# Performance work log

Measured on AMD Instinct MI355X. Metric: run time of the kernel, lower is better.

## Reference

```python
import jax, jax.numpy as jnp
import numpy as np

NUM_HEADS = 12


def setup_inputs() -> dict:
    key = jax.random.key(0)
    k1, k2, k3 = jax.random.split(key, 3)
    B, T, N, D = 8, 8, 196, 768
    x = jax.random.normal(k1, (B, T * N, D), dtype=jnp.float32)
    w_qkv = jax.random.normal(k2, (D, 3 * D), dtype=jnp.float32) * 0.02
    w_proj = jax.random.normal(k3, (D, D), dtype=jnp.float32) * 0.02
    b_proj = jnp.zeros((D,), dtype=jnp.float32)
    return {"x": x, "T": T, "N": N, "w_qkv": w_qkv, "w_proj": w_proj, "b_proj": b_proj}


def reference(x, T, N, w_qkv, w_proj, b_proj):
    B, TN, D = x.shape
    H = NUM_HEADS
    hd = D // H
    scale = hd ** -0.5
    # qkv projection: (B, TN, 3, H, hd)
    qkv = (x @ w_qkv).reshape(B, TN, 3, H, hd)
    # -> (3, B, H, T, N, hd)
    qkv = jnp.transpose(qkv, (2, 0, 3, 1, 4)).reshape(3, B, H, T, N, hd)
    q, k, v = qkv[0], qkv[1], qkv[2]

    # Temporal branch: mean-pool over spatial axis N (keepdim -> length-1 attn axis)
    q_t = q.mean(axis=3, keepdims=True)            # (B,H,T,1,hd)
    k_t = k.mean(axis=3, keepdims=True)            # (B,H,T,1,hd)
    v_t = v.mean(axis=3, keepdims=True)            # (B,H,T,1,hd)
    attn_t = jnp.einsum('bhtqd,bhtkd->bhtqk', q_t, k_t) * scale  # (B,H,T,1,1)
    attn_t = jax.nn.softmax(attn_t, axis=-1)
    x_t = jnp.einsum('bhtqk,bhtkd->bhtqd', attn_t, v_t)[:, :, :, 0]  # (B,H,T,hd)

    # Spatial branch: full attention within each frame
    attn_s = jnp.einsum('bhtnd,bhtmd->bhtnm', q, k) * scale  # (B,H,T,N,N)
    attn_s = jax.nn.softmax(attn_s, axis=-1)
    x_s = jnp.einsum('bhtnm,bhtmd->bhtnd', attn_s, v)        # (B,H,T,N,hd)

    # Combine: broadcast temporal result over spatial positions, add
    out = x_s + x_t[:, :, :, None, :]                        # (B,H,T,N,hd)
    out = out.reshape(B, H, T * N, hd)
    out = jnp.transpose(out, (0, 2, 1, 3)).reshape(B * T * N, D)
    return out @ w_proj + b_proj
```

## Files before the change

kernel.cpp:

```cpp
#include <hip/hip_runtime.h>
#include <math.h>

#define BB 8
#define TT 8
#define NN 196
#define DD 768
#define HH 12
#define HD 64
#define TN (TT * NN)
#define MM (BB * TN)
#define D3 (3 * DD)

typedef _Float16 f16;
typedef _Float16 f16x8 __attribute__((ext_vector_type(8)));
typedef _Float16 f16x4 __attribute__((ext_vector_type(4)));
typedef float f32x4 __attribute__((ext_vector_type(4)));
typedef unsigned int u32;

#define GLDS16(gp, lp)                                                        \
  __builtin_amdgcn_global_load_lds(                                           \
      (const __attribute__((address_space(1))) u32*)(gp),                     \
      (__attribute__((address_space(3))) u32*)(lp), 16, 0, 0)

#define MFMA16(a, b, c) __builtin_amdgcn_mfma_f32_16x16x32_f16(a, b, c, 0, 0, 0)
#define SBAR() __builtin_amdgcn_s_barrier()
#define SCHED() __builtin_amdgcn_sched_barrier(0)
#define PBAR()  do { SCHED(); SBAR(); SCHED(); } while (0)

#define GK DD
#define GNT 12

template <int MI0, int NJ0>
__device__ __forceinline__ void quad(f32x4 (&acc)[8][4],
                                     const f16x8 (&af)[4][2],
                                     const f16x8 (&bf)[2][2]) {
  __builtin_amdgcn_s_setprio(1);
#pragma unroll
  for (int i = 0; i < 4; i++)
#pragma unroll
    for (int j = 0; j < 2; j++) {
      acc[MI0 + i][NJ0 + j] = MFMA16(af[i][0], bf[j][0], acc[MI0 + i][NJ0 + j]);
      acc[MI0 + i][NJ0 + j] = MFMA16(af[i][1], bf[j][1], acc[MI0 + i][NJ0 + j]);
    }
  __builtin_amdgcn_s_setprio(0);
}

__global__ __launch_bounds__(512, 2) void gemm256_qkv(
    const f16* __restrict__ A, const f16* __restrict__ Bt,
    f16* __restrict__ C16) {
  __shared__ f16 As[2 * 256 * 64];
  __shared__ f16 Bs[2 * 256 * 64];

  const int nwg = 49 * 9;
  const int orig = blockIdx.x;
  const int xcd = orig & 7;
  const int inner = orig >> 3;
  const int qq = nwg >> 3;
  const int rr = nwg & 7;
  const int swzid =
      ((xcd < rr) ? xcd * (qq + 1) : rr * (qq + 1) + (xcd - rr) * qq) + inner;
  const int bm = (swzid / 9) * 256;
  const int bn = (swzid % 9) * 256;

  const int tid = threadIdx.x;
  const int lane = tid & 63;
  const int wave = tid >> 6;
  const int wy = wave >> 2;
  const int wx = wave & 3;
  const int m = lane & 15;
  const int q = lane >> 4;

  const int sr = tid >> 3;
  const int sc = (tid & 7) ^ (sr & 7);
  const f16* gA = A + (size_t)(bm + sr) * GK + sc * 8;
  const f16* gB = Bt + (size_t)(bn + sr) * GK + sc * 8;
  f16* lA = &As[tid * 8];
  f16* lB = &Bs[tid * 8];

#define STAGE_A(db, h, tile)                                   \
  do {                                                         \
    const f16* _s = gA + (size_t)(h) * 128 * GK + (tile) * 64; \
    f16* _d = lA + (db) * 16384 + (h) * 8192;                  \
    GLDS16(_s, _d);                                            \
    GLDS16(_s + 64 * GK, _d + 4096);                           \
  } while (0)
#define STAGE_B(db, h, tile)                                   \
  do {                                                         \
    const f16* _s = gB + (size_t)(h) * 128 * GK + (tile) * 64; \
    f16* _d = lB + (db) * 16384 + (h) * 8192;                  \
    GLDS16(_s, _d);                                            \
    GLDS16(_s + 64 * GK, _d + 4096);                           \
  } while (0)

  const int sw = m & 7;
  const int c0 = (q ^ sw) * 8;
  const int c1 = ((q + 4) ^ sw) * 8;
  const f16* rA = &As[(wy * 128 + m) * 64];
  const f16* rB = &Bs[(wx * 64 + m) * 64];

  STAGE_A(0, 0, 0);
  STAGE_A(0, 1, 0);
  STAGE_B(0, 0, 0);
  STAGE_B(0, 1, 0);
  STAGE_B(1, 0, 1);
  STAGE_B(1, 1, 1);

  f32x4 acc[8][4];
#pragma unroll
  for (int i = 0; i < 8; i++)
#pragma unroll
    for (int j = 0; j < 4; j++) acc[i][j] = (f32x4)0.0f;

  SCHED();
  asm volatile("s_waitcnt vmcnt(4)" ::: "memory");
  SCHED();
  SBAR();
  SCHED();

#pragma unroll 2
  for (int t = 0; t < GNT; ++t) {
    const int db = t & 1;
    const f16* pA = rA + db * 16384;
    const f16* pB = rB + db * 16384;
    const int tA = (t + 1 < GNT) ? t + 1 : GNT - 1;
    const int tB = (t + 2 < GNT) ? t + 2 : GNT - 1;

    f16x8 af[4][2], bf0[2][2], bf1[2][2];

#pragma unroll
    for (int i = 0; i < 4; i++) {
      af[i][0] = *(const f16x8*)(pA + i * 1024 + c0);
      af[i][1] = *(const f16x8*)(pA + i * 1024 + c1);
    }
#pragma unroll
    for (int j = 0; j < 2; j++) {
      bf0[j][0] = *(const f16x8*)(pB + j * 1024 + c0);
      bf0[j][1] = *(const f16x8*)(pB + j * 1024 + c1);
    }
    STAGE_A(db ^ 1, 0, tA);
    PBAR();
    quad<0, 0>(acc, af, bf0);
    PBAR();

#pragma unroll
    for (int j = 0; j < 2; j++) {
      bf1[j][0] = *(const f16x8*)(pB + (2 + j) * 1024 + c0);
      bf1[j][1] = *(const f16x8*)(pB + (2 + j) * 1024 + c1);
    }
    STAGE_A(db ^ 1, 1, tA);
    PBAR();
    quad<0, 2>(acc, af, bf1);
    PBAR();

#pragma unroll
    for (int i = 0; i < 4; i++) {
      af[i][0] = *(const f16x8*)(pA + (4 + i) * 1024 + c0);
      af[i][1] = *(const f16x8*)(pA + (4 + i) * 1024 + c1);
    }
    STAGE_B(db, 0, tB);
    PBAR();
    quad<4, 2>(acc, af, bf1);
    PBAR();

    STAGE_B(db, 1, tB);
    SCHED();
    asm volatile("s_waitcnt vmcnt(4)" ::: "memory");
    PBAR();
    quad<4, 0>(acc, af, bf0);
    PBAR();
  }

  const int col0 = bn + wx * 64;
#pragma unroll
  for (int mi = 0; mi < 8; mi++) {
    const int row0 = bm + wy * 128 + mi * 16 + q * 4;
#pragma unroll
    for (int r = 0; r < 4; r++) {
      const int token = row0 + r;
      const int f = token / NN;
      const int n = token - f * NN;
      f16* fb = C16 + ((size_t)f * (HH * 3)) * (NN * 64) + n * 64;
#pragma unroll
      for (int ni = 0; ni < 4; ni++) {
        const int col = col0 + ni * 16 + m;
        const int qt = col / DD;
        const int rem = col - qt * DD;
        const int hh = rem >> 6;
        const int d = rem & 63;
        fb[(size_t)(hh * 3 + qt) * (NN * 64) + d] = (f16)acc[mi][ni][r];
      }
    }
  }
#undef STAGE_A
#undef STAGE_B
}

__global__ __launch_bounds__(256) void gemm_f16nt(
    const f16* __restrict__ A, const f16* __restrict__ Bt,
    float* __restrict__ C32, f16* __restrict__ C16, int K, int Ncol,
    const float* __restrict__ bias, int mode) {
  __shared__ f16 As[128 * 64];
  __shared__ f16 Bs[128 * 64];

  const int tid = threadIdx.x;
  const int lane = tid & 63;
  const int wave = tid >> 6;
  const int wy = wave >> 1, wx = wave & 1;
  const int bm = blockIdx.y * 128;
  const int bn = blockIdx.x * 128;

  const f16* aP[4];
  const f16* bP[4];
#pragma unroll
  for (int it = 0; it < 4; it++) {
    int ci = tid + it * 256;
    int r = ci >> 3;
    int c = (ci & 7) ^ (r & 7);
    aP[it] = A + (size_t)(bm + r) * K + c * 8;
    bP[it] = Bt + (size_t)(bn + r) * K + c * 8;
  }

  f32x4 acc[4][4];
#pragma unroll
  for (int i = 0; i < 4; i++)
#pragma unroll
    for (int j = 0; j < 4; j++) acc[i][j] = (f32x4)0.0f;

  const int fr = lane & 15;
  const int q = lane >> 4;
  const int sw = fr & 7;

  for (int kt = 0; kt < K; kt += 64) {
#pragma unroll
    for (int it = 0; it < 4; it++) {
      GLDS16(aP[it] + kt, &As[(tid + it * 256) * 8]);
      GLDS16(bP[it] + kt, &Bs[(tid + it * 256) * 8]);
    }
    __syncthreads();

#pragma unroll
    for (int kk = 0; kk < 2; kk++) {
      const int lc = ((kk * 4 + q) ^ sw) * 8;
      f16x8 af[4], bf[4];
#pragma unroll
      for (int mi = 0; mi < 4; mi++)
        af[mi] = *(const f16x8*)&As[(wy * 64 + mi * 16 + fr) * 64 + lc];
#pragma unroll
      for (int ni = 0; ni < 4; ni++)
        bf[ni] = *(const f16x8*)&Bs[(wx * 64 + ni * 16 + fr) * 64 + lc];

#pragma unroll
      for (int mi = 0; mi < 4; mi++)
#pragma unroll
        for (int ni = 0; ni < 4; ni++)
          acc[mi][ni] = MFMA16(af[mi], bf[ni], acc[mi][ni]);
    }
    __syncthreads();
  }

  if (mode == 0) {
#pragma unroll
    for (int mi = 0; mi < 4; mi++) {
      const int row0 = bm + wy * 64 + mi * 16 + (lane >> 4) * 4;
#pragma unroll
      for (int ni = 0; ni < 4; ni++) {
        const int col = bn + wx * 64 + ni * 16 + (lane & 15);
        float bv = (bias != nullptr) ? bias[col] : 0.0f;
#pragma unroll
        for (int r = 0; r < 4; r++)
          C32[(size_t)(row0 + r) * Ncol + col] = acc[mi][ni][r] + bv;
      }
    }
  } else {
#pragma unroll
    for (int mi = 0; mi < 4; mi++) {
      const int row0 = bm + wy * 64 + mi * 16 + (lane >> 4) * 4;
#pragma unroll
      for (int r = 0; r < 4; r++) {
        const int token = row0 + r;
        const int f = token / NN;
        const int n = token - f * NN;
        f16* fb = C16 + ((size_t)f * (HH * 3) * NN) * 64 + n * 64;
#pragma unroll
        for (int ni = 0; ni < 4; ni++) {
          const int col = bn + wx * 64 + ni * 16 + (lane & 15);
          const int qt = col / DD;
          const int rem = col - qt * DD;
          const int hh = rem >> 6;
          const int d = rem & 63;
          fb[(size_t)(hh * 3 + qt) * NN * 64 + d] = (f16)acc[mi][ni][r];
        }
      }
    }
  }
}

__global__ __launch_bounds__(256) void conv_f32_to_f16(
    const float* __restrict__ in, f16* __restrict__ out, int n4) {
  int i = blockIdx.x * blockDim.x + threadIdx.x;
  const int stride = gridDim.x * blockDim.x;
  for (; i < n4; i += stride) {
    float4 f = ((const float4*)in)[i];
    f16x4 h;
    h[0] = (f16)f.x;
    h[1] = (f16)f.y;
    h[2] = (f16)f.z;
    h[3] = (f16)f.w;
    ((f16x4*)out)[i] = h;
  }
}

__global__ __launch_bounds__(256) void transpose_f32_to_f16(
    const float* __restrict__ W, f16* __restrict__ Wt, int K, int Ncol) {
  __shared__ float tileS[32][33];
  const int k0 = blockIdx.y * 32, n0 = blockIdx.x * 32;
  const int tx = threadIdx.x & 31, ty = threadIdx.x >> 5;
#pragma unroll
  for (int i = 0; i < 4; i++)
    tileS[ty + i * 8][tx] = W[(size_t)(k0 + ty + i * 8) * Ncol + n0 + tx];
  __syncthreads();
#pragma unroll
  for (int i = 0; i < 4; i++)
    Wt[(size_t)(n0 + ty + i * 8) * K + k0 + tx] = (f16)tileS[tx][ty + i * 8];
}

#define VSTR 232

__global__ __launch_bounds__(512, 4) void attn_mfma(
    const f16* __restrict__ qkv, f16* __restrict__ out) {
  __shared__ f16 KS[196 * 64];
  __shared__ f16 VS[64 * VSTR];
  __shared__ __align__(16) f16 PS[8 * 16 * 40];
  __shared__ float vmean[64];
  float* red = (float*)PS;

  const int bi = blockIdx.x;
  const int t = bi % TT;
  const int h = (bi / TT) % HH;
  const int b = bi / (TT * HH);
  const int frame = b * TT + t;
  const int tok0 = frame * NN;

  const f16* Qb = qkv + (size_t)(frame * HH + h) * 3 * NN * 64;
  const f16* Kb = Qb + NN * 64;
  const f16* Vb = Qb + 2 * NN * 64;

  const int tid = threadIdx.x;
  const int lane = tid & 63;
  const int wave = tid >> 6;
  const int m = lane & 15;
  const int q = lane >> 4;

#pragma unroll
  for (int it = 0; it < 3; it++) {
    int chunk = tid + it * 512;
    int row = chunk >> 3, pc = chunk & 7;
    int c = pc ^ (row & 7);
    GLDS16(Kb + row * 64 + c * 8, &KS[chunk * 8]);
  }
  if (tid < 32) {
    int chunk = 1536 + tid;
    int row = chunk >> 3, pc = chunk & 7;
    int c = pc ^ (row & 7);
    *(f16x8*)&KS[chunk * 8] = *(const f16x8*)(Kb + row * 64 + c * 8);
  }

  for (int idx = tid; idx < 64 * 9; idx += 512) {
    int d = idx / 9, c = idx % 9;
    *(f16x4*)&VS[d * VSTR + 196 + c * 4] = (f16x4){0, 0, 0, 0};
  }

  const int vd = tid & 63;
  const int kb = tid >> 6;
  float vpart = 0.0f;
  if (kb < 7) {
#pragma unroll
    for (int it = 0; it < 7; it++) {
      int k0 = kb * 28 + it * 4;
      f16x4 pk;
#pragma unroll
      for (int j = 0; j < 4; j++) {
        f16 v = Vb[(k0 + j) * 64 + vd];
        pk[j] = v;
        vpart += (float)v;
      }
      *(f16x4*)&VS[vd * VSTR + k0] = pk;
    }
  }
  red[tid] = vpart;
  __syncthreads();
  if (tid < 64) {
    float s = 0.0f;
#pragma unroll
    for (int g = 0; g < 8; g++) s += red[tid + 64 * g];
    vmean[tid] = s * (1.0f / (float)NN);
  }
  __syncthreads();

  f16* PSw = &PS[wave * 640];

  for (int qt = wave; qt < 13; qt += 8) {
    const int q0 = qt * 16;
    int qrow = q0 + m;
    if (qrow > NN - 1) qrow = NN - 1;
    const f16* qbase = Qb + qrow * 64;
    f16x8 aq0 = *(const f16x8*)(qbase + q * 8);
    f16x8 aq1 = *(const f16x8*)(qbase + 32 + q * 8);

    f32x4 o0 = (f32x4)0.0f, o1 = (f32x4)0.0f, o2 = (f32x4)0.0f,
          o3 = (f32x4)0.0f;
    float l[4] = {0.0f, 0.0f, 0.0f, 0.0f};

    for (int ch = 0; ch < 7; ch++) {
      const int keyA = ch * 32 + m;
      const int keyB = keyA + 16;
      const int kA = keyA > 195 ? 195 : keyA;
      const int kB = keyB > 195 ? 195 : keyB;
      const int swA = kA & 7, swB = kB & 7;
      f16x8 b00 = *(const f16x8*)&KS[kA * 64 + ((q ^ swA) * 8)];
      f16x8 b01 = *(const f16x8*)&KS[kA * 64 + (((q + 4) ^ swA) * 8)];
      f16x8 b10 = *(const f16x8*)&KS[kB * 64 + ((q ^ swB) * 8)];
      f16x8 b11 = *(const f16x8*)&KS[kB * 64 + (((q + 4) ^ swB) * 8)];
      f32x4 z = (f32x4)0.0f;
      f32x4 s0 = MFMA16(aq0, b00, z);
      s0 = MFMA16(aq1, b01, s0);
      f32x4 s1 = MFMA16(aq0, b10, z);
      s1 = MFMA16(aq1, b11, s1);

      const bool v0 = keyA < NN;
      const bool v1 = keyB < NN;
#pragma unroll
      for (int r = 0; r < 4; r++) {
        float p0 = v0 ? __expf(s0[r] * 0.125f) : 0.0f;
        float p1 = v1 ? __expf(s1[r] * 0.125f) : 0.0f;
        l[r] += p0 + p1;
        PSw[(q * 4 + r) * 40 + m] = (f16)p0;
        PSw[(q * 4 + r) * 40 + 16 + m] = (f16)p1;
      }
      f16x8 pa = *(const f16x8*)&PSw[m * 40 + q * 8];
      f16x8 bv0 = *(const f16x8*)&VS[(0 * 16 + m) * VSTR + ch * 32 + q * 8];
      f16x8 bv1 = *(const f16x8*)&VS[(1 * 16 + m) * VSTR + ch * 32 + q * 8];
      f16x8 bv2 = *(const f16x8*)&VS[(2 * 16 + m) * VSTR + ch * 32 + q * 8];
      f16x8 bv3 = *(const f16x8*)&VS[(3 * 16 + m) * VSTR + ch * 32 + q * 8];
      o0 = MFMA16(pa, bv0, o0);
      o1 = MFMA16(pa, bv1, o1);
      o2 = MFMA16(pa, bv2, o2);
      o3 = MFMA16(pa, bv3, o3);
    }

#pragma unroll
    for (int r = 0; r < 4; r++) {
      float s = l[r];
      s += __shfl_xor(s, 1);
      s += __shfl_xor(s, 2);
      s += __shfl_xor(s, 4);
      s += __shfl_xor(s, 8);
      l[r] = 1.0f / s;
    }

#pragma unroll
    for (int r = 0; r < 4; r++) {
      const int query = q0 + q * 4 + r;
      if (query < NN) {
        f16* orow = out + (size_t)(tok0 + query) * DD + h * HD;
        orow[m] = (f16)(o0[r] * l[r] + vmean[m]);
        orow[16 + m] = (f16)(o1[r] * l[r] + vmean[16 + m]);
        orow[32 + m] = (f16)(o2[r] * l[r] + vmean[32 + m]);
        orow[48 + m] = (f16)(o3[r] * l[r] + vmean[48 + m]);
      }
    }
  }
}

extern "C" void kernel_launch(void* const* d_in, const int* in_sizes, int n_in,
                              void* d_out, int out_size, void* d_ws,
                              size_t ws_size, hipStream_t stream) {
  (void)in_sizes;
  (void)n_in;
  (void)out_size;
  (void)ws_size;
  const float* x      = (const float*)d_in[0];
  const float* w_qkv  = (const float*)d_in[3];
  const float* w_proj = (const float*)d_in[4];
  const float* b_proj = (const float*)d_in[5];
  float* out = (float*)d_out;

  char* ws = (char*)d_ws;
  f16* qkvh = (f16*)ws;
  f16* xh = (f16*)(ws + (size_t)MM * D3 * 2);
  f16* wqkvT = xh + (size_t)MM * DD;
  f16* wprojT = wqkvT + (size_t)D3 * DD;

  conv_f32_to_f16<<<2048, 256, 0, stream>>>(x, xh, MM * DD / 4);
  transpose_f32_to_f16<<<dim3(D3 / 32, DD / 32), 256, 0, stream>>>(w_qkv,
                                                                   wqkvT, DD, D3);
  transpose_f32_to_f16<<<dim3(DD / 32, DD / 32), 256, 0, stream>>>(w_proj,
                                                                   wprojT, DD, DD);
  gemm256_qkv<<<dim3(49 * 9), 512, 0, stream>>>(xh, wqkvT, qkvh);
  attn_mfma<<<BB * HH * TT, 512, 0, stream>>>(qkvh, xh);
  gemm_f16nt<<<dim3(DD / 128, MM / 128), 256, 0, stream>>>(
      xh, wprojT, out, nullptr, DD, DD, b_proj, 0);
}
```

Baseline: 215.0 us.

## Fuse fp32-to-fp16 conversion of x into QKV GEMM A-tile staging

Removes the separate conversion kernel that turned x into fp16. The QKV GEMM now reads fp32 x straight into registers, converts it to fp16 and writes it into swizzled LDS. The B tiles still use direct global-to-LDS loads. This saves one full read and write pass over x and one launch, at the cost of more register pressure, manual waitcnt choreography, and fp32 A loads that re-read x for each of the 9 column tiles at double the bytes.

Measured after the change: 230.9 us. 7.4% more time.

```diff
diff --git a/kernel.cpp b/kernel.cpp
--- a/kernel.cpp
+++ b/kernel.cpp
@@ -27,6 +27,13 @@
 #define SCHED() __builtin_amdgcn_sched_barrier(0)
 #define PBAR()  do { SCHED(); SBAR(); SCHED(); } while (0)
 
+__device__ __forceinline__ f16x8 cvt8(f32x4 a, f32x4 b) {
+  f16x8 r;
+  r[0] = (f16)a[0]; r[1] = (f16)a[1]; r[2] = (f16)a[2]; r[3] = (f16)a[3];
+  r[4] = (f16)b[0]; r[5] = (f16)b[1]; r[6] = (f16)b[2]; r[7] = (f16)b[3];
+  return r;
+}
+
 #define GK DD
 #define GNT 12
 
@@ -46,7 +53,7 @@
 }
 
 __global__ __launch_bounds__(512, 2) void gemm256_qkv(
-    const f16* __restrict__ A, const f16* __restrict__ Bt,
+    const float* __restrict__ A, const f16* __restrict__ Bt,
     f16* __restrict__ C16) {
   __shared__ f16 As[2 * 256 * 64];
   __shared__ f16 Bs[2 * 256 * 64];
@@ -72,24 +79,31 @@
 
   const int sr = tid >> 3;
   const int sc = (tid & 7) ^ (sr & 7);
-  const f16* gA = A + (size_t)(bm + sr) * GK + sc * 8;
+  const float* gA = A + (size_t)(bm + sr) * GK + sc * 8;
   const f16* gB = Bt + (size_t)(bn + sr) * GK + sc * 8;
   f16* lA = &As[tid * 8];
   f16* lB = &Bs[tid * 8];
 
-#define STAGE_A(db, h, tile)                                   \
-  do {                                                         \
-    const f16* _s = gA + (size_t)(h) * 128 * GK + (tile) * 64; \
-    f16* _d = lA + (db) * 16384 + (h) * 8192;                  \
-    GLDS16(_s, _d);                                            \
-    GLDS16(_s + 64 * GK, _d + 4096);                           \
+#define LOAD_A(dst, h, tile)                                       \
+  do {                                                             \
+    const float* _s = gA + (size_t)(h) * 128 * GK + (tile) * 64;   \
+    dst[0] = *(const f32x4*)(_s);                                  \
+    dst[1] = *(const f32x4*)(_s + 4);                              \
+    dst[2] = *(const f32x4*)(_s + 64 * GK);                        \
+    dst[3] = *(const f32x4*)(_s + 64 * GK + 4);                    \
   } while (0)
-#define STAGE_B(db, h, tile)                                   \
-  do {                                                         \
-    const f16* _s = gB + (size_t)(h) * 128 * GK + (tile) * 64; \
-    f16* _d = lB + (db) * 16384 + (h) * 8192;                  \
-    GLDS16(_s, _d);                                            \
-    GLDS16(_s + 64 * GK, _d + 4096);                           \
+#define WRITE_A(src, db_, h)                                       \
+  do {                                                             \
+    f16* _d = lA + (db_) * 16384 + (h) * 8192;                     \
+    *(f16x8*)(_d) = cvt8(src[0], src[1]);                          \
+    *(f16x8*)(_d + 4096) = cvt8(src[2], src[3]);                   \
+  } while (0)
+#define STAGE_B(db_, h, tile)                                      \
+  do {                                                             \
+    const f16* _s = gB + (size_t)(h) * 128 * GK + (tile) * 64;     \
+    f16* _d = lB + (db_) * 16384 + (h) * 8192;                     \
+    GLDS16(_s, _d);                                                \
+    GLDS16(_s + 64 * GK, _d + 4096);                               \
   } while (0)
 
   const int sw = m & 7;
@@ -98,8 +112,9 @@
   const f16* rA = &As[(wy * 128 + m) * 64];
   const f16* rB = &Bs[(wx * 64 + m) * 64];
 
-  STAGE_A(0, 0, 0);
-  STAGE_A(0, 1, 0);
+  f32x4 pa0[4], pa1[4];
+  LOAD_A(pa0, 0, 0);
+  LOAD_A(pa1, 1, 0);
   STAGE_B(0, 0, 0);
   STAGE_B(0, 1, 0);
   STAGE_B(1, 0, 1);
@@ -112,7 +127,12 @@
     for (int j = 0; j < 4; j++) acc[i][j] = (f32x4)0.0f;
 
   SCHED();
-  asm volatile("s_waitcnt vmcnt(4)" ::: "memory");
+  asm volatile("s_waitcnt vmcnt(8)" ::: "memory");
+  SCHED();
+  WRITE_A(pa0, 0, 0);
+  WRITE_A(pa1, 0, 1);
+  SCHED();
+  asm volatile("s_waitcnt vmcnt(4) lgkmcnt(0)" ::: "memory");
   SCHED();
   SBAR();
   SCHED();
@@ -126,7 +146,9 @@
     const int tB = (t + 2 < GNT) ? t + 2 : GNT - 1;
 
     f16x8 af[4][2], bf0[2][2], bf1[2][2];
-
+    f32x4 L0[4], L1[4];
+
+    LOAD_A(L0, 0, tA);
 #pragma unroll
     for (int i = 0; i < 4; i++) {
       af[i][0] = *(const f16x8*)(pA + i * 1024 + c0);
@@ -137,27 +159,30 @@
       bf0[j][0] = *(const f16x8*)(pB + j * 1024 + c0);
       bf0[j][1] = *(const f16x8*)(pB + j * 1024 + c1);
     }
-    STAGE_A(db ^ 1, 0, tA);
     PBAR();
     quad<0, 0>(acc, af, bf0);
     PBAR();
 
+    LOAD_A(L1, 1, tA);
 #pragma unroll
     for (int j = 0; j < 2; j++) {
       bf1[j][0] = *(const f16x8*)(pB + (2 + j) * 1024 + c0);
       bf1[j][1] = *(const f16x8*)(pB + (2 + j) * 1024 + c1);
     }
-    STAGE_A(db ^ 1, 1, tA);
     PBAR();
     quad<0, 2>(acc, af, bf1);
     PBAR();
 
+    STAGE_B(db, 0, tB);
 #pragma unroll
     for (int i = 0; i < 4; i++) {
       af[i][0] = *(const f16x8*)(pA + (4 + i) * 1024 + c0);
       af[i][1] = *(const f16x8*)(pA + (4 + i) * 1024 + c1);
     }
-    STAGE_B(db, 0, tB);
+    SCHED();
+    asm volatile("s_waitcnt vmcnt(6)" ::: "memory");
+    SCHED();
+    WRITE_A(L0, db ^ 1, 0);
     PBAR();
     quad<4, 2>(acc, af, bf1);
     PBAR();
@@ -165,8 +190,12 @@
     STAGE_B(db, 1, tB);
     SCHED();
     asm volatile("s_waitcnt vmcnt(4)" ::: "memory");
+    SCHED();
+    WRITE_A(L1, db ^ 1, 1);
     PBAR();
     quad<4, 0>(acc, af, bf0);
+    SCHED();
+    asm volatile("s_waitcnt lgkmcnt(0)" ::: "memory");
     PBAR();
   }
 
@@ -191,7 +220,8 @@
       }
     }
   }
-#undef STAGE_A
+#undef LOAD_A
+#undef WRITE_A
 #undef STAGE_B
 }
 
@@ -292,21 +322,6 @@
         }
       }
     }
-  }
-}
-
-__global__ __launch_bounds__(256) void conv_f32_to_f16(
-    const float* __restrict__ in, f16* __restrict__ out, int n4) {
-  int i = blockIdx.x * blockDim.x + threadIdx.x;
-  const int stride = gridDim.x * blockDim.x;
-  for (; i < n4; i += stride) {
-    float4 f = ((const float4*)in)[i];
-    f16x4 h;
-    h[0] = (f16)f.x;
-    h[1] = (f16)f.y;
-    h[2] = (f16)f.z;
-    h[3] = (f16)f.w;
-    ((f16x4*)out)[i] = h;
   }
 }
 
@@ -491,12 +506,11 @@
   f16* wqkvT = xh + (size_t)MM * DD;
   f16* wprojT = wqkvT + (size_t)D3 * DD;
 
-  conv_f32_to_f16<<<2048, 256, 0, stream>>>(x, xh, MM * DD / 4);
   transpose_f32_to_f16<<<dim3(D3 / 32, DD / 32), 256, 0, stream>>>(w_qkv,
                                                                    wqkvT, DD, D3);
   transpose_f32_to_f16<<<dim3(DD / 32, DD / 32), 256, 0, stream>>>(w_proj,
                                                                    wprojT, DD, DD);
-  gemm256_qkv<<<dim3(49 * 9), 512, 0, stream>>>(xh, wqkvT, qkvh);
+  gemm256_qkv<<<dim3(49 * 9), 512, 0, stream>>>(x, wqkvT, qkvh);
   attn_mfma<<<BB * HH * TT, 512, 0, stream>>>(qkvh, xh);
   gemm_f16nt<<<dim3(DD / 128, MM / 128), 256, 0, stream>>>(
       xh, wprojT, out, nullptr, DD, DD, b_proj, 0);
```
